# Kernel tuning notes

Measured on AMD Instinct MI355X. Metric: run time of the kernel, lower is better.

Reference implementation:

```python
import jax, jax.numpy as jnp
import numpy as np
import math

D_MODEL = 1024
NUM_HEADS = 16
D_K = D_MODEL // NUM_HEADS  # 64
B, S = 4, 2048


def setup_inputs() -> dict:
    key = jax.random.key(0)
    ks = jax.random.split(key, 9)
    sc = 1.0 / math.sqrt(D_MODEL)
    return {
        "x": jax.random.normal(ks[0], (B, S, D_MODEL), jnp.float32),
        "Wq": jax.random.normal(ks[1], (D_MODEL, D_MODEL), jnp.float32) * sc,
        "bq": jax.random.normal(ks[2], (D_MODEL,), jnp.float32) * 0.01,
        "Wk": jax.random.normal(ks[3], (D_MODEL, D_MODEL), jnp.float32) * sc,
        "bk": jax.random.normal(ks[4], (D_MODEL,), jnp.float32) * 0.01,
        "Wv": jax.random.normal(ks[5], (D_MODEL, D_MODEL), jnp.float32) * sc,
        "bv": jax.random.normal(ks[6], (D_MODEL,), jnp.float32) * 0.01,
        "Wo": jax.random.normal(ks[7], (D_MODEL, D_MODEL), jnp.float32) * sc,
        "bo": jax.random.normal(ks[8], (D_MODEL,), jnp.float32) * 0.01,
    }


def reference(x, Wq, bq, Wk, bk, Wv, bv, Wo, bo):
    b, s, d = x.shape
    # Linear projections (torch Linear: x @ W.T + b)
    Q = x @ Wq.T + bq
    K = x @ Wk.T + bk
    V = x @ Wv.T + bv
    # [b, s, h*d_k] -> [b, h, s, d_k]
    split = lambda t: t.reshape(b, s, NUM_HEADS, D_K).transpose(0, 2, 1, 3)
    Q, K, V = split(Q), split(K), split(V)
    # Causal mask: query i can attend to keys j <= i
    seq = jnp.arange(s)
    causal = seq[:, None] >= seq[None, :]  # [s, s]
    # Scaled dot-product attention
    scores = jnp.einsum('bhqd,bhkd->bhqk', Q, K) / math.sqrt(D_K)
    scores = jnp.where(causal, scores, -jnp.inf)
    weights = jax.nn.softmax(scores, axis=-1)
    attn = jnp.einsum('bhqk,bhkd->bhqd', weights, V)
    # [b, h, s, d_v] -> [b, s, h*d_v]
    attn = attn.transpose(0, 2, 1, 3).reshape(b, s, NUM_HEADS * D_K)
    return attn @ Wo.T + bo
```

## Files before the change

### kernel.cpp

```cpp
#include <hip/hip_runtime.h>
#include <hip/hip_bf16.h>


typedef unsigned short u16;
typedef unsigned int u32;
typedef __attribute__((ext_vector_type(2))) unsigned int uint2v;
typedef __attribute__((ext_vector_type(4))) short short4v;
typedef __attribute__((ext_vector_type(8))) short short8;
typedef __attribute__((ext_vector_type(4))) float f32x4;

#define KDIM   1024
#define S_LEN  2048
#define NHEADS 16
#define DK     64
#define NEG_BIG (-30000.0f)
#define QSCALE 0.18033688011112043f

__device__ __forceinline__ u16 f2bf(float f) {
  unsigned u = __float_as_uint(f);
  return (u16)((u + 0x7FFFu + ((u >> 16) & 1u)) >> 16);
}
__device__ __forceinline__ u32 pkbf(float a, float b) {
  u32 ua = __float_as_uint(a) + 0x8000u;
  u32 ub = __float_as_uint(b) + 0x8000u;
  return __builtin_amdgcn_perm(ub, ua, 0x07060302u);
}
__device__ __forceinline__ void gl_lds16(const u16* g, u16* l) {
  __builtin_amdgcn_global_load_lds((const __attribute__((address_space(1))) void*)g,
                                   (__attribute__((address_space(3))) void*)l, 16, 0, 0);
}

__global__ __launch_bounds__(256) void cvt_kernel(
    const float* __restrict__ x,  const float* __restrict__ Wq,
    const float* __restrict__ Wk, const float* __restrict__ Wv,
    u16* __restrict__ xb, u16* __restrict__ wqb,
    u16* __restrict__ wkb, u16* __restrict__ wvb) {
  const int NX = 2097152, NW = 262144;
  const int total = NX + 3 * NW;
  for (int i = blockIdx.x * 256 + threadIdx.x; i < total; i += gridDim.x * 256) {
    const float* src; u16* dst; int off;
    if (i < NX)               { src = x;  dst = xb;  off = i; }
    else if (i < NX + NW)     { src = Wq; dst = wqb; off = i - NX; }
    else if (i < NX + 2 * NW) { src = Wk; dst = wkb; off = i - NX - NW; }
    else                      { src = Wv; dst = wvb; off = i - NX - 2 * NW; }
    f32x4 v = *(const f32x4*)(src + (size_t)off * 4);
    short4v o;
    o[0] = (short)f2bf(v[0]); o[1] = (short)f2bf(v[1]);
    o[2] = (short)f2bf(v[2]); o[3] = (short)f2bf(v[3]);
    *(short4v*)(dst + (size_t)off * 4) = o;
  }
}

__global__ __launch_bounds__(256) void cvt_wo(const float* __restrict__ W,
                                              u16* __restrict__ out) {
  const int i = blockIdx.x * 256 + threadIdx.x;
  f32x4 v = *(const f32x4*)(W + (size_t)i * 4);
  short4v o;
  o[0] = (short)f2bf(v[0]); o[1] = (short)f2bf(v[1]);
  o[2] = (short)f2bf(v[2]); o[3] = (short)f2bf(v[3]);
  *(short4v*)(out + (size_t)i * 4) = o;
}

template <int MODE>
__device__ __forceinline__ void gemm_body(const u16* __restrict__ A,
                                          const u16* __restrict__ B,
                                          const float* __restrict__ bias,
                                          void* __restrict__ outv) {
  extern __shared__ __align__(16) u16 smem[];
  u16* As0 = smem;
  u16* As1 = smem + 4096;
  u16* Bs0 = smem + 8192;
  u16* Bs1 = smem + 12288;
  const int tid = threadIdx.x;
  const int wave = tid >> 6, lane = tid & 63;
  const int quad = lane >> 4, l16 = lane & 15;
  const int wy = wave >> 1, wx = wave & 1;
  const int m0 = blockIdx.x * 128, n0 = blockIdx.y * 128;

  f32x4 acc[4][4];
#pragma unroll
  for (int i = 0; i < 4; i++)
#pragma unroll
    for (int j = 0; j < 4; j++) acc[i][j] = (f32x4){0.f, 0.f, 0.f, 0.f};

  const int srow = wave * 16 + (lane >> 2);
  const int scol = (lane & 3) * 8;
  const u16* gA0 = A + (size_t)(m0 + srow) * KDIM + scol;
  const u16* gA1 = gA0 + (size_t)64 * KDIM;
  const u16* gB0 = B + (size_t)(n0 + srow) * KDIM + scol;
  const u16* gB1 = gB0 + (size_t)64 * KDIM;
  const int soff = srow * 32 + scol;

  for (int k = 0; k < KDIM; k += 64) {
    __syncthreads();
    gl_lds16(gA0 + k,      &As0[soff]);
    gl_lds16(gA0 + k + 32, &As1[soff]);
    gl_lds16(gA1 + k,      &As0[soff + 2048]);
    gl_lds16(gA1 + k + 32, &As1[soff + 2048]);
    gl_lds16(gB0 + k,      &Bs0[soff]);
    gl_lds16(gB0 + k + 32, &Bs1[soff]);
    gl_lds16(gB1 + k,      &Bs0[soff + 2048]);
    gl_lds16(gB1 + k + 32, &Bs1[soff + 2048]);
    __syncthreads();
#pragma unroll
    for (int h = 0; h < 2; h++) {
      const u16* Ap = h ? As1 : As0;
      const u16* Bp = h ? Bs1 : Bs0;
      short8 af[4], bfr[4];
#pragma unroll
      for (int i = 0; i < 4; i++)
        af[i] = *(const short8*)&Ap[(wy * 64 + i * 16 + l16) * 32 + quad * 8];
#pragma unroll
      for (int j = 0; j < 4; j++)
        bfr[j] = *(const short8*)&Bp[(wx * 64 + j * 16 + l16) * 32 + quad * 8];
#pragma unroll
      for (int i = 0; i < 4; i++)
#pragma unroll
        for (int j = 0; j < 4; j++) {
          if (MODE == 2)
            acc[i][j] = __builtin_amdgcn_mfma_f32_16x16x32_bf16(af[i], bfr[j], acc[i][j], 0, 0, 0);
          else
            acc[i][j] = __builtin_amdgcn_mfma_f32_16x16x32_bf16(bfr[j], af[i], acc[i][j], 0, 0, 0);
        }
    }
  }

  if (MODE == 0 || MODE == 1) {
#pragma unroll
    for (int j = 0; j < 4; j++) {
      const int colb = n0 + wx * 64 + j * 16 + quad * 4;
      const int h = colb >> 6, d0 = colb & 63;
      const f32x4 bv4 = *(const f32x4*)&bias[colb];
#pragma unroll
      for (int i = 0; i < 4; i++) {
        const int row = m0 + wy * 64 + i * 16 + l16;
        const int b = row >> 11, s = row & 2047;
        float v0 = acc[i][j][0] + bv4[0], v1 = acc[i][j][1] + bv4[1];
        float v2 = acc[i][j][2] + bv4[2], v3 = acc[i][j][3] + bv4[3];
        if (MODE == 0) { v0 *= QSCALE; v1 *= QSCALE; v2 *= QSCALE; v3 *= QSCALE; }
        uint2v pk = {pkbf(v0, v1), pkbf(v2, v3)};
        *(uint2v*)&((u16*)outv)[(((size_t)(b * NHEADS + h)) * S_LEN + s) * DK + d0] = pk;
      }
    }
  } else if (MODE == 2) {
#pragma unroll
    for (int j = 0; j < 4; j++) {
      const int col = n0 + wx * 64 + j * 16 + l16;
      const int h = col >> 6, d = col & 63;
      const float bvs = bias[col];
#pragma unroll
      for (int i = 0; i < 4; i++) {
        const int rowb = m0 + wy * 64 + i * 16 + quad * 4;
        const int b = rowb >> 11, s0 = rowb & 2047;
        uint2v pk = {pkbf(acc[i][j][0] + bvs, acc[i][j][1] + bvs),
                     pkbf(acc[i][j][2] + bvs, acc[i][j][3] + bvs)};
        *(uint2v*)&((u16*)outv)[(((size_t)(b * NHEADS + h)) * DK + d) * S_LEN + s0] = pk;
      }
    }
  } else {
#pragma unroll
    for (int j = 0; j < 4; j++) {
      const int colb = n0 + wx * 64 + j * 16 + quad * 4;
      const f32x4 bv4 = *(const f32x4*)&bias[colb];
#pragma unroll
      for (int i = 0; i < 4; i++) {
        const int row = m0 + wy * 64 + i * 16 + l16;
        f32x4 v = {acc[i][j][0] + bv4[0], acc[i][j][1] + bv4[1],
                   acc[i][j][2] + bv4[2], acc[i][j][3] + bv4[3]};
        *(f32x4*)&((float*)outv)[(size_t)row * 1024 + colb] = v;
      }
    }
  }
}

__global__ __launch_bounds__(256) void qkv_gemm(
    const u16* __restrict__ xb,
    const u16* __restrict__ wqb, const float* __restrict__ bq,
    const u16* __restrict__ wkb, const float* __restrict__ bk,
    const u16* __restrict__ wvb, const float* __restrict__ bv,
    u16* __restrict__ qb, u16* __restrict__ kb, u16* __restrict__ vb) {
  if (blockIdx.z == 0)      gemm_body<0>(xb, wqb, bq, qb);
  else if (blockIdx.z == 1) gemm_body<1>(xb, wkb, bk, kb);
  else                      gemm_body<2>(xb, wvb, bv, vb);
}

__global__ __launch_bounds__(256) void out_gemm(const u16* __restrict__ A,
                                                const u16* __restrict__ wob,
                                                const float* __restrict__ bo,
                                                float* __restrict__ out) {
  gemm_body<3>(A, wob, bo, out);
}

__global__ __launch_bounds__(256) void attn_kernel(const u16* __restrict__ Qb,
                                                   const u16* __restrict__ Kb,
                                                   const u16* __restrict__ Vb,
                                                   u16* __restrict__ Ob) {
  __shared__ __align__(16) u16 Ks0[64 * 32];
  __shared__ __align__(16) u16 Ks1[64 * 32];
  __shared__ __align__(16) u16 Vt0[64 * 32];
  __shared__ __align__(16) u16 Vt1[64 * 32];
  __shared__ __align__(16) u16 Ps[4 * 16 * 72];
  const int bh = blockIdx.x;
  const int qt = (int)gridDim.y - 1 - (int)blockIdx.y;
  const int tid = threadIdx.x, wave = tid >> 6, lane = tid & 63;
  const int quad = lane >> 4, l16 = lane & 15;
  const u16* Qh = Qb + (size_t)bh * S_LEN * DK;
  const u16* Kh = Kb + (size_t)bh * S_LEN * DK;
  const u16* Vh = Vb + (size_t)bh * S_LEN * DK;

  const int qrow = qt * 64 + wave * 16 + l16;
  const short8 qf0 = *(const short8*)&Qh[(size_t)qrow * DK + quad * 8];
  const short8 qf1 = *(const short8*)&Qh[(size_t)qrow * DK + 32 + quad * 8];

  short8 ones;
#pragma unroll
  for (int i = 0; i < 8; i++) ones[i] = (short)0x3F80;

  f32x4 o[4];
#pragma unroll
  for (int j = 0; j < 4; j++) o[j] = (f32x4){0.f, 0.f, 0.f, 0.f};
  f32x4 l_acc = (f32x4){0.f, 0.f, 0.f, 0.f};

  const int sr = lane >> 2, sc = lane & 3;
  u16* dK0 = &Ks0[wave * 512 + lane * 8];
  u16* dK1 = &Ks1[wave * 512 + lane * 8];
  u16* dV0 = &Vt0[wave * 512 + lane * 8];
  u16* dV1 = &Vt1[wave * 512 + lane * 8];
  const u16* gK = Kh + (size_t)(wave * 16 + sr) * DK + sc * 8;
  const u16* gV = Vh + (size_t)(wave * 16 + sr) * S_LEN + sc * 8;

  const int qrow_acc = qt * 64 + wave * 16 + quad * 4;
  u16* Pw = &Ps[wave * 16 * 72];

  for (int t = 0; t <= qt; ++t) {
    const int kbase = t * 64;
    __syncthreads();
    gl_lds16(gK + (size_t)kbase * DK, dK0);
    gl_lds16(gK + (size_t)kbase * DK + 32, dK1);
    gl_lds16(gV + kbase, dV0);
    gl_lds16(gV + kbase + 32, dV1);
    __syncthreads();

    f32x4 st[4];
#pragma unroll
    for (int j = 0; j < 4; j++) {
      short8 ka0 = *(const short8*)&Ks0[(j * 16 + l16) * 32 + quad * 8];
      short8 ka1 = *(const short8*)&Ks1[(j * 16 + l16) * 32 + quad * 8];
      f32x4 c = (f32x4){0.f, 0.f, 0.f, 0.f};
      c = __builtin_amdgcn_mfma_f32_16x16x32_bf16(ka0, qf0, c, 0, 0, 0);
      c = __builtin_amdgcn_mfma_f32_16x16x32_bf16(ka1, qf1, c, 0, 0, 0);
      st[j] = c;
    }

    if (t == qt) {
#pragma unroll
      for (int j = 0; j < 4; j++) {
        const int keyb = kbase + j * 16 + quad * 4;
#pragma unroll
        for (int r = 0; r < 4; r++)
          st[j][r] = (keyb + r > qrow) ? NEG_BIG : st[j][r];
      }
    }

#pragma unroll
    for (int j = 0; j < 4; j++) {
      float e0 = exp2f(st[j][0]), e1 = exp2f(st[j][1]);
      float e2 = exp2f(st[j][2]), e3 = exp2f(st[j][3]);
      uint2v pk = {pkbf(e0, e1), pkbf(e2, e3)};
      *(uint2v*)&Pw[l16 * 72 + j * 16 + quad * 4] = pk;
    }
    const short8 pa0 = *(const short8*)&Pw[l16 * 72 + quad * 8];
    const short8 pa1 = *(const short8*)&Pw[l16 * 72 + 32 + quad * 8];
    l_acc = __builtin_amdgcn_mfma_f32_16x16x32_bf16(pa0, ones, l_acc, 0, 0, 0);
    l_acc = __builtin_amdgcn_mfma_f32_16x16x32_bf16(pa1, ones, l_acc, 0, 0, 0);
#pragma unroll
    for (int jd = 0; jd < 4; jd++) {
      short8 vb0 = *(const short8*)&Vt0[(jd * 16 + l16) * 32 + quad * 8];
      short8 vb1 = *(const short8*)&Vt1[(jd * 16 + l16) * 32 + quad * 8];
      o[jd] = __builtin_amdgcn_mfma_f32_16x16x32_bf16(pa0, vb0, o[jd], 0, 0, 0);
      o[jd] = __builtin_amdgcn_mfma_f32_16x16x32_bf16(pa1, vb1, o[jd], 0, 0, 0);
    }
  }

  const int b = bh >> 4, h = bh & 15;
  float inv[4];
#pragma unroll
  for (int r = 0; r < 4; r++) inv[r] = __builtin_amdgcn_rcpf(l_acc[r]);
#pragma unroll
  for (int jd = 0; jd < 4; jd++) {
    const int col = h * DK + jd * 16 + l16;
#pragma unroll
    for (int r = 0; r < 4; r++) {
      const int s = qrow_acc + r;
      float v = o[jd][r] * inv[r];
      unsigned u = __float_as_uint(v) + 0x8000u;
      Ob[((size_t)b * S_LEN + s) * 1024 + col] = (u16)(u >> 16);
    }
  }
}

extern "C" void kernel_launch(void* const* d_in, const int* in_sizes, int n_in,
                              void* d_out, int out_size, void* d_ws, size_t ws_size,
                              hipStream_t stream) {
  const float* x  = (const float*)d_in[0];
  const float* Wq = (const float*)d_in[1];
  const float* bq = (const float*)d_in[2];
  const float* Wk = (const float*)d_in[3];
  const float* bk = (const float*)d_in[4];
  const float* Wv = (const float*)d_in[5];
  const float* bv = (const float*)d_in[6];
  const float* Wo = (const float*)d_in[7];
  const float* bo = (const float*)d_in[8];

  u16* outh = (u16*)d_out;
  u16* wsh  = (u16*)d_ws;
  u16* qb  = outh;
  u16* xb  = outh + (size_t)8388608;
  u16* kb  = wsh;
  u16* vb  = wsh + (size_t)8388608;
  u16* ab  = wsh + (size_t)16777216;
  u16* wqb = ab;
  u16* wkb = wqb + (size_t)1048576;
  u16* wvb = wkb + (size_t)1048576;
  u16* wob = kb;

  cvt_kernel<<<dim3(2048), 256, 0, stream>>>(x, Wq, Wk, Wv, xb, wqb, wkb, wvb);
  qkv_gemm<<<dim3(64, 8, 3), 256, 32768, stream>>>(xb, wqb, bq, wkb, bk, wvb, bv, qb, kb, vb);
  attn_kernel<<<dim3(64, 32), 256, 0, stream>>>(qb, kb, vb, ab);
  cvt_wo<<<dim3(1024), 256, 0, stream>>>(Wo, wob);
  out_gemm<<<dim3(64, 8), 256, 32768, stream>>>(ab, wob, bo, (float*)d_out);
}
```

Measured before the change: 262.8 us.

## Rewrite attention with 32x32 MFMA, 128-query tiles and pre-tiled K/V layouts

The attention kernel moves from 16x16x32 to 32x32x16 bf16 MFMA, with each wave handling 32 query rows and each block 128 queries, which halves the grid. The QKV GEMM epilogue now writes K and V in a pre-tiled layout so each attention tile can be loaded into LDS with contiguous 16-byte copies. P fragments are rearranged in registers with permlane32_swap instead of going through a shared-memory round trip. The aim is less LDS traffic, fewer instructions per FLOP and more reuse of each K/V tile. The cost is fewer blocks, which may cause load imbalance on the causal triangle, plus higher register pressure.

Result: faster. 250.5 us (-4.7%).

```diff
diff --git a/kernel.cpp b/kernel.cpp
--- a/kernel.cpp
+++ b/kernel.cpp
@@ -5,9 +5,11 @@
 typedef unsigned short u16;
 typedef unsigned int u32;
 typedef __attribute__((ext_vector_type(2))) unsigned int uint2v;
+typedef __attribute__((ext_vector_type(4))) unsigned int uint4v;
 typedef __attribute__((ext_vector_type(4))) short short4v;
 typedef __attribute__((ext_vector_type(8))) short short8;
 typedef __attribute__((ext_vector_type(4))) float f32x4;
+typedef __attribute__((ext_vector_type(16))) float f32x16;
 
 #define KDIM   1024
 #define S_LEN  2048
@@ -139,7 +141,12 @@
         float v2 = acc[i][j][2] + bv4[2], v3 = acc[i][j][3] + bv4[3];
         if (MODE == 0) { v0 *= QSCALE; v1 *= QSCALE; v2 *= QSCALE; v3 *= QSCALE; }
         uint2v pk = {pkbf(v0, v1), pkbf(v2, v3)};
-        *(uint2v*)&((u16*)outv)[(((size_t)(b * NHEADS + h)) * S_LEN + s) * DK + d0] = pk;
+        if (MODE == 0) {
+          *(uint2v*)&((u16*)outv)[(((size_t)(b * NHEADS + h)) * S_LEN + s) * DK + d0] = pk;
+        } else {
+          *(uint2v*)&((u16*)outv)[((((size_t)(b * NHEADS + h)) * 32 + (s >> 6)) * 8 +
+                                   (d0 >> 3)) * 512 + (s & 63) * 8 + (d0 & 7)] = pk;
+        }
       }
     }
   } else if (MODE == 2) {
@@ -154,7 +161,8 @@
         const int b = rowb >> 11, s0 = rowb & 2047;
         uint2v pk = {pkbf(acc[i][j][0] + bvs, acc[i][j][1] + bvs),
                      pkbf(acc[i][j][2] + bvs, acc[i][j][3] + bvs)};
-        *(uint2v*)&((u16*)outv)[(((size_t)(b * NHEADS + h)) * DK + d) * S_LEN + s0] = pk;
+        *(uint2v*)&((u16*)outv)[((((size_t)(b * NHEADS + h)) * 32 + (s0 >> 6)) * 8 +
+                                 ((s0 >> 3) & 7)) * 512 + (size_t)d * 8 + (s0 & 7)] = pk;
       }
     }
   } else {
@@ -195,107 +203,108 @@
                                                    const u16* __restrict__ Kb,
                                                    const u16* __restrict__ Vb,
                                                    u16* __restrict__ Ob) {
-  __shared__ __align__(16) u16 Ks0[64 * 32];
-  __shared__ __align__(16) u16 Ks1[64 * 32];
-  __shared__ __align__(16) u16 Vt0[64 * 32];
-  __shared__ __align__(16) u16 Vt1[64 * 32];
-  __shared__ __align__(16) u16 Ps[4 * 16 * 72];
+  __shared__ __align__(16) u16 Ks[2][8][512];
+  __shared__ __align__(16) u16 Vs[2][8][512];
   const int bh = blockIdx.x;
   const int qt = (int)gridDim.y - 1 - (int)blockIdx.y;
   const int tid = threadIdx.x, wave = tid >> 6, lane = tid & 63;
-  const int quad = lane >> 4, l16 = lane & 15;
+  const int l32 = lane & 31, hi = lane >> 5;
   const u16* Qh = Qb + (size_t)bh * S_LEN * DK;
-  const u16* Kh = Kb + (size_t)bh * S_LEN * DK;
-  const u16* Vh = Vb + (size_t)bh * S_LEN * DK;
-
-  const int qrow = qt * 64 + wave * 16 + l16;
-  const short8 qf0 = *(const short8*)&Qh[(size_t)qrow * DK + quad * 8];
-  const short8 qf1 = *(const short8*)&Qh[(size_t)qrow * DK + 32 + quad * 8];
+  const u16* Kg = Kb + (size_t)bh * S_LEN * DK;
+  const u16* Vg = Vb + (size_t)bh * S_LEN * DK;
+  const int qw = qt * 128 + wave * 32;
+  const int qrow = qw + l32;
+
+  short8 qf[4];
+#pragma unroll
+  for (int c = 0; c < 4; c++)
+    qf[c] = *(const short8*)&Qh[(size_t)qrow * DK + c * 16 + hi * 8];
 
   short8 ones;
 #pragma unroll
   for (int i = 0; i < 8; i++) ones[i] = (short)0x3F80;
 
-  f32x4 o[4];
-#pragma unroll
-  for (int j = 0; j < 4; j++) o[j] = (f32x4){0.f, 0.f, 0.f, 0.f};
-  f32x4 l_acc = (f32x4){0.f, 0.f, 0.f, 0.f};
-
-  const int sr = lane >> 2, sc = lane & 3;
-  u16* dK0 = &Ks0[wave * 512 + lane * 8];
-  u16* dK1 = &Ks1[wave * 512 + lane * 8];
-  u16* dV0 = &Vt0[wave * 512 + lane * 8];
-  u16* dV1 = &Vt1[wave * 512 + lane * 8];
-  const u16* gK = Kh + (size_t)(wave * 16 + sr) * DK + sc * 8;
-  const u16* gV = Vh + (size_t)(wave * 16 + sr) * S_LEN + sc * 8;
-
-  const int qrow_acc = qt * 64 + wave * 16 + quad * 4;
-  u16* Pw = &Ps[wave * 16 * 72];
+  f32x16 zz;
+#pragma unroll
+  for (int i = 0; i < 16; i++) zz[i] = 0.f;
+  f32x16 o0 = zz, o1 = zz, l_acc = zz;
+
+  const int sg = wave * 2;
+  const u16* srcK = Kg + sg * 512 + lane * 8;
+  const u16* srcV = Vg + sg * 512 + lane * 8;
+  u16* dstK0 = &Ks[0][sg][lane * 8];
+  u16* dstK1 = &Ks[1][sg][lane * 8];
+  u16* dstV0 = &Vs[0][sg][lane * 8];
+  u16* dstV1 = &Vs[1][sg][lane * 8];
 
   for (int t = 0; t <= qt; ++t) {
-    const int kbase = t * 64;
+    const size_t g0 = (size_t)(2 * t) * 4096, g1 = (size_t)(2 * t + 1) * 4096;
     __syncthreads();
-    gl_lds16(gK + (size_t)kbase * DK, dK0);
-    gl_lds16(gK + (size_t)kbase * DK + 32, dK1);
-    gl_lds16(gV + kbase, dV0);
-    gl_lds16(gV + kbase + 32, dV1);
+    gl_lds16(srcK + g0, dstK0);        gl_lds16(srcK + g0 + 512, dstK0 + 512);
+    gl_lds16(srcK + g1, dstK1);        gl_lds16(srcK + g1 + 512, dstK1 + 512);
+    gl_lds16(srcV + g0, dstV0);        gl_lds16(srcV + g0 + 512, dstV0 + 512);
+    gl_lds16(srcV + g1, dstV1);        gl_lds16(srcV + g1 + 512, dstV1 + 512);
     __syncthreads();
 
-    f32x4 st[4];
-#pragma unroll
-    for (int j = 0; j < 4; j++) {
-      short8 ka0 = *(const short8*)&Ks0[(j * 16 + l16) * 32 + quad * 8];
-      short8 ka1 = *(const short8*)&Ks1[(j * 16 + l16) * 32 + quad * 8];
-      f32x4 c = (f32x4){0.f, 0.f, 0.f, 0.f};
-      c = __builtin_amdgcn_mfma_f32_16x16x32_bf16(ka0, qf0, c, 0, 0, 0);
-      c = __builtin_amdgcn_mfma_f32_16x16x32_bf16(ka1, qf1, c, 0, 0, 0);
-      st[j] = c;
-    }
-
-    if (t == qt) {
-#pragma unroll
-      for (int j = 0; j < 4; j++) {
-        const int keyb = kbase + j * 16 + quad * 4;
-#pragma unroll
-        for (int r = 0; r < 4; r++)
-          st[j][r] = (keyb + r > qrow) ? NEG_BIG : st[j][r];
-      }
-    }
-
-#pragma unroll
-    for (int j = 0; j < 4; j++) {
-      float e0 = exp2f(st[j][0]), e1 = exp2f(st[j][1]);
-      float e2 = exp2f(st[j][2]), e3 = exp2f(st[j][3]);
-      uint2v pk = {pkbf(e0, e1), pkbf(e2, e3)};
-      *(uint2v*)&Pw[l16 * 72 + j * 16 + quad * 4] = pk;
-    }
-    const short8 pa0 = *(const short8*)&Pw[l16 * 72 + quad * 8];
-    const short8 pa1 = *(const short8*)&Pw[l16 * 72 + 32 + quad * 8];
-    l_acc = __builtin_amdgcn_mfma_f32_16x16x32_bf16(pa0, ones, l_acc, 0, 0, 0);
-    l_acc = __builtin_amdgcn_mfma_f32_16x16x32_bf16(pa1, ones, l_acc, 0, 0, 0);
-#pragma unroll
-    for (int jd = 0; jd < 4; jd++) {
-      short8 vb0 = *(const short8*)&Vt0[(jd * 16 + l16) * 32 + quad * 8];
-      short8 vb1 = *(const short8*)&Vt1[(jd * 16 + l16) * 32 + quad * 8];
-      o[jd] = __builtin_amdgcn_mfma_f32_16x16x32_bf16(pa0, vb0, o[jd], 0, 0, 0);
-      o[jd] = __builtin_amdgcn_mfma_f32_16x16x32_bf16(pa1, vb1, o[jd], 0, 0, 0);
+#pragma unroll
+    for (int kb = 0; kb < 4; ++kb) {
+      const int kbase = t * 128 + kb * 32;
+      if (kbase > qw) break;
+
+      f32x16 st = zz;
+#pragma unroll
+      for (int c = 0; c < 4; c++) {
+        const short8 kf = *(const short8*)
+            &Ks[kb >> 1][c * 2 + hi][((kb & 1) * 32 + l32) * 8];
+        st = __builtin_amdgcn_mfma_f32_32x32x16_bf16(kf, qf[c], st, 0, 0, 0);
+      }
+
+      if (kbase == qw) {
+#pragma unroll
+        for (int r = 0; r < 16; r++) {
+          const int ko = (r & 3) + 8 * (r >> 2) + 4 * hi;
+          st[r] = (ko > l32) ? NEG_BIG : st[r];
+        }
+      }
+
+      float e[16];
+#pragma unroll
+      for (int r = 0; r < 16; r++) e[r] = exp2f(st[r]);
+
+      uint2v sA0 = __builtin_amdgcn_permlane32_swap(pkbf(e[0], e[1]),  pkbf(e[4], e[5]),  false, false);
+      uint2v sB0 = __builtin_amdgcn_permlane32_swap(pkbf(e[2], e[3]),  pkbf(e[6], e[7]),  false, false);
+      uint2v sA1 = __builtin_amdgcn_permlane32_swap(pkbf(e[8], e[9]),  pkbf(e[12], e[13]), false, false);
+      uint2v sB1 = __builtin_amdgcn_permlane32_swap(pkbf(e[10], e[11]), pkbf(e[14], e[15]), false, false);
+      union { uint4v u; short8 s; } p0, p1;
+      p0.u = (uint4v){sA0[0], sB0[0], sA0[1], sB0[1]};
+      p1.u = (uint4v){sA1[0], sB1[0], sA1[1], sB1[1]};
+      const short8 pa0 = p0.s, pa1 = p1.s;
+
+      l_acc = __builtin_amdgcn_mfma_f32_32x32x16_bf16(pa0, ones, l_acc, 0, 0, 0);
+      l_acc = __builtin_amdgcn_mfma_f32_32x32x16_bf16(pa1, ones, l_acc, 0, 0, 0);
+
+#pragma unroll
+      for (int cc = 0; cc < 2; cc++) {
+        const int kc = kb * 2 + cc;
+        const short8 pa = cc ? pa1 : pa0;
+        const short8 vf0 = *(const short8*)&Vs[kc >> 2][(kc & 3) * 2 + hi][l32 * 8];
+        const short8 vf1 = *(const short8*)&Vs[kc >> 2][(kc & 3) * 2 + hi][(32 + l32) * 8];
+        o0 = __builtin_amdgcn_mfma_f32_32x32x16_bf16(pa, vf0, o0, 0, 0, 0);
+        o1 = __builtin_amdgcn_mfma_f32_32x32x16_bf16(pa, vf1, o1, 0, 0, 0);
+      }
     }
   }
 
   const int b = bh >> 4, h = bh & 15;
-  float inv[4];
-#pragma unroll
-  for (int r = 0; r < 4; r++) inv[r] = __builtin_amdgcn_rcpf(l_acc[r]);
-#pragma unroll
-  for (int jd = 0; jd < 4; jd++) {
-    const int col = h * DK + jd * 16 + l16;
-#pragma unroll
-    for (int r = 0; r < 4; r++) {
-      const int s = qrow_acc + r;
-      float v = o[jd][r] * inv[r];
-      unsigned u = __float_as_uint(v) + 0x8000u;
-      Ob[((size_t)b * S_LEN + s) * 1024 + col] = (u16)(u >> 16);
-    }
+#pragma unroll
+  for (int r = 0; r < 16; r++) {
+    const int s = qw + (r & 3) + 8 * (r >> 2) + 4 * hi;
+    const float inv = __builtin_amdgcn_rcpf(l_acc[r]);
+    const unsigned v0 = __float_as_uint(o0[r] * inv) + 0x8000u;
+    const unsigned v1 = __float_as_uint(o1[r] * inv) + 0x8000u;
+    u16* p = &Ob[((size_t)b * S_LEN + s) * 1024 + h * DK + l32];
+    p[0]  = (u16)(v0 >> 16);
+    p[32] = (u16)(v1 >> 16);
   }
 }
 
@@ -326,7 +335,7 @@
 
   cvt_kernel<<<dim3(2048), 256, 0, stream>>>(x, Wq, Wk, Wv, xb, wqb, wkb, wvb);
   qkv_gemm<<<dim3(64, 8, 3), 256, 32768, stream>>>(xb, wqb, bq, wkb, bk, wvb, bv, qb, kb, vb);
-  attn_kernel<<<dim3(64, 32), 256, 0, stream>>>(qb, kb, vb, ab);
+  attn_kernel<<<dim3(64, 16), 256, 0, stream>>>(qb, kb, vb, ab);
   cvt_wo<<<dim3(1024), 256, 0, stream>>>(Wo, wob);
   out_gemm<<<dim3(64, 8), 256, 32768, stream>>>(ab, wob, bo, (float*)d_out);
 }
```
